# Optimization experiments

Hardware: AMD Instinct MI355X
Metric: run time of the kernel (lower is better)

Reference implementation:

```python
import jax, jax.numpy as jnp
import numpy as np

B, S, L, C, H, D, CP = 32, 4, 64, 32, 4, 8, 16  # batch, tracks, bins, c_msa, heads, d_head, c_pair


def _ln(x, g, b, eps=1e-5):
    m = jnp.mean(x, axis=-1, keepdims=True)
    v = jnp.mean((x - m) ** 2, axis=-1, keepdims=True)
    return (x - m) / jnp.sqrt(v + eps) * g + b


def setup_inputs() -> dict:
    key = jax.random.key(0)
    ks = jax.random.split(key, 20)
    n = lambda k, shape, s=0.1: jax.random.normal(k, shape, jnp.float32) * s
    return dict(
        chip_ctcf=n(ks[0], (B, L), 1.0),
        chip_hac=n(ks[1], (B, L), 1.0),
        chip_me1=n(ks[2], (B, L), 1.0),
        chip_me3=n(ks[3], (B, L), 1.0),
        bulk_map=n(ks[4], (B, 1, L, L), 1.0),
        we_w=n(ks[5], (C, 1)), we_b=jnp.zeros((C,), jnp.float32),
        pos=n(ks[6], (1, 1, L, C)),
        mn_g=jnp.ones((C,), jnp.float32), mn_b=jnp.zeros((C,), jnp.float32),
        wq=n(ks[7], (C, C)), bq=jnp.zeros((C,), jnp.float32),
        wk=n(ks[8], (C, C)), bk=jnp.zeros((C,), jnp.float32),
        wv=n(ks[9], (C, C)), bv=jnp.zeros((C,), jnp.float32),
        wo=n(ks[10], (C, C)), bo=jnp.zeros((C,), jnp.float32),
        an_g=jnp.ones((C,), jnp.float32), an_b=jnp.zeros((C,), jnp.float32),
        conv_w=n(ks[11], (H,)), conv_b=jnp.zeros((H,), jnp.float32),
        gate_w=n(ks[12], (H, D, D)), gate_b=jnp.zeros((H, D), jnp.float32),
        pp_w=n(ks[13], (CP, C * C), 0.03), pp_b=jnp.zeros((CP,), jnp.float32),
        ada_g=jnp.ones((CP,), jnp.float32), ada_b=jnp.zeros((CP,), jnp.float32),
        ada_alpha=jnp.ones((1,), jnp.float32),
    )


def reference(chip_ctcf, chip_hac, chip_me1, chip_me3, bulk_map,
              we_w, we_b, pos, mn_g, mn_b,
              wq, bq, wk, bk, wv, bv, wo, bo, an_g, an_b,
              conv_w, conv_b, gate_w, gate_b,
              pp_w, pp_b, ada_g, ada_b, ada_alpha):
    # 1) build MSA: (B, S=4, L, C)
    signals = jnp.stack([chip_ctcf, chip_hac, chip_me1, chip_me3], axis=1)  # (B,S,L)
    msa = signals[..., None] * we_w[:, 0] + we_b                            # Linear(1,C)
    x = _ln(msa + pos, mn_g, mn_b)                                          # (B,S,L,C)

    # 2) row self-attention with bulk-derived per-head bias
    q = (x @ wq.T + bq).reshape(B, S, L, H, D)
    k = (x @ wk.T + bk).reshape(B, S, L, H, D)
    v = (x @ wv.T + bv).reshape(B, S, L, H, D)
    scores = jnp.einsum('bslhd,bsmhd->bshlm', q, k) / jnp.sqrt(jnp.float32(D))
    bias = bulk_map * conv_w.reshape(1, H, 1, 1) + conv_b.reshape(1, H, 1, 1)  # 1x1 conv -> (B,H,L,L)
    attn = jax.nn.softmax(scores + bias[:, None], axis=-1)                     # (B,S,H,L,L)
    out = jnp.einsum('bshlm,bsmhd->bshld', attn, v)
    gate = jax.nn.sigmoid(jnp.einsum('hcd,bshld->bshlc', gate_w, out)
                          + gate_b[None, None, :, None, :])
    out = out * gate
    out = out.transpose(0, 1, 3, 2, 4).reshape(B, S, L, C)
    out = out @ wo.T + bo
    x = _ln(x + out, an_g, an_b)                                            # post-attn LayerNorm

    # 3) outer-product (of max over tracks) pair features
    m = jnp.max(x, axis=1)                                                  # (B,L,C)
    pair = jnp.einsum('bic,bjd->bijcd', m, m).reshape(B, L, L, C * C)       # (B,L,L,1024)
    nrm = jnp.sqrt(jnp.sum(pair * pair, axis=-1, keepdims=True))
    pair = pair / jnp.maximum(nrm, 1e-6)                                    # F.normalize
    feat = pair @ pp_w.T + pp_b                                             # (B,L,L,CP)
    feat = feat + ada_alpha * _ln(feat, ada_g, ada_b)                       # AdaNorm
    feat = jax.nn.silu(feat)
    return feat.transpose(0, 3, 1, 2)                                       # (B,CP,L,L)
```

## Files before the change

kernel.cpp:

```cpp
#include <hip/hip_runtime.h>
#include <hip/hip_bf16.h>

#define NB 32
#define NS 4
#define NL 64
#define NC 32
#define NH 4
#define ND 8
#define NCP 16

using fp = const float* __restrict__;

__global__ __launch_bounds__(512) void k1_attn(
    fp ctcf, fp hac, fp me1, fp me3, fp bulk,
    fp we_w, fp we_b, fp pos, fp mn_g, fp mn_b,
    fp wq, fp bq, fp wk, fp bk, fp wv, fp bv,
    fp wo, fp bo, fp an_g, fp an_b,
    fp conv_w, fp conv_b, fp gate_w, fp gate_b,
    float* __restrict__ xpostT)
{
    __shared__ __align__(16) float q2[NL*36];
    __shared__ __align__(16) float k2[NL*36];
    __shared__ __align__(16) float v2[NL*36];
    __shared__ __align__(16) float x2[NL*36];
    __shared__ __align__(16) float a2[NL*36];
    __shared__ float bs[32*65];
    __shared__ __align__(16) float ws_wq[NC*NC];
    __shared__ __align__(16) float ws_wk[NC*NC];
    __shared__ __align__(16) float ws_wv[NC*NC];
    __shared__ __align__(16) float ws_wo[NC*NC];
    __shared__ __align__(16) float ws_gw[NH*ND*ND];
    __shared__ __align__(16) float ws_par[352];

    const int t    = threadIdx.x;
    const int w    = t >> 6;
    const int l    = t & 63;
    const int bx   = blockIdx.x;
    const int b    = bx >> 3;
    const int s    = (bx >> 1) & 3;
    const int half = bx & 1;

    if (t < 256) ((float4*)ws_wq)[t]       = ((const float4*)wq)[t];
    else         ((float4*)ws_wk)[t - 256] = ((const float4*)wk)[t - 256];

    if (t < 256) ((float4*)ws_wv)[t] = ((const float4*)wv)[t];
    else {
        int u = t - 256;
        if (u < 64) ((float4*)ws_gw)[u] = ((const float4*)gate_w)[u];
        else if (u < 152){
            int p = u - 64;
            const float* sp = (p < 8)  ? we_w : (p < 16) ? we_b
                            : (p < 24) ? mn_g : (p < 32) ? mn_b
                            : (p < 40) ? bq   : (p < 48) ? bk
                            : (p < 56) ? bv   : (p < 64) ? bo
                            : (p < 72) ? an_g : (p < 80) ? an_b : gate_b;
            ((float4*)ws_par)[p] = ((const float4*)sp)[p & 7];
        }
    }
    if (t < 256){
        int c = t >> 3, k4 = t & 7;
        ((float4*)ws_wo)[c*8 + (k4 ^ ((c >> 1) & 7))] = ((const float4*)wo)[t];
    }
    {
        float4 v = ((const float4*)(bulk + b*NL*NL + half*32*NL))[t];
        int row = t >> 4, col = (t & 15) << 2;
        float* dst = &bs[row*65 + col];
        dst[0] = v.x; dst[1] = v.y; dst[2] = v.z; dst[3] = v.w;
    }

    fp sigp = (s == 0) ? ctcf : (s == 1) ? hac : (s == 2) ? me1 : me3;
    const float sig = sigp[b*NL + l];
    __syncthreads();

    const float4* pws = (const float4*)ws_par;

    float x[NC];
    float mean = 0.f;
#pragma unroll
    for (int k4 = 0; k4 < 8; k4++){
        float4 ww = pws[k4];
        float4 wb = pws[8 + k4];
        float4 pp = ((const float4*)pos)[l*8 + k4];
        x[4*k4+0] = sig*ww.x + wb.x + pp.x;
        x[4*k4+1] = sig*ww.y + wb.y + pp.y;
        x[4*k4+2] = sig*ww.z + wb.z + pp.z;
        x[4*k4+3] = sig*ww.w + wb.w + pp.w;
        mean += x[4*k4+0] + x[4*k4+1] + x[4*k4+2] + x[4*k4+3];
    }
    mean *= (1.f/NC);
    float var = 0.f;
#pragma unroll
    for (int c = 0; c < NC; c++){ float d = x[c] - mean; var += d*d; }
    var *= (1.f/NC);
    float inv = rsqrtf(var + 1e-5f);
#pragma unroll
    for (int k4 = 0; k4 < 8; k4++){
        float4 gg = pws[16 + k4];
        float4 bb = pws[24 + k4];
        x[4*k4+0] = (x[4*k4+0] - mean)*inv*gg.x + bb.x;
        x[4*k4+1] = (x[4*k4+1] - mean)*inv*gg.y + bb.y;
        x[4*k4+2] = (x[4*k4+2] - mean)*inv*gg.z + bb.z;
        x[4*k4+3] = (x[4*k4+3] - mean)*inv*gg.w + bb.w;
    }

    float aqv[4], akv[4], avv[4];
#pragma unroll
    for (int e4 = 0; e4 < 4; e4++){
        const int e = (w << 2) + e4;
        float aq = ws_par[128 + e], ak = ws_par[160 + e], av = ws_par[192 + e];
#pragma unroll
        for (int k4 = 0; k4 < 8; k4++){
            float4 wq4 = *(const float4*)&ws_wq[e*NC + 4*k4];
            float4 wk4 = *(const float4*)&ws_wk[e*NC + 4*k4];
            float4 wv4 = *(const float4*)&ws_wv[e*NC + 4*k4];
            float x0 = x[4*k4+0], x1 = x[4*k4+1], x2v = x[4*k4+2], x3 = x[4*k4+3];
            aq += wq4.x*x0 + wq4.y*x1 + wq4.z*x2v + wq4.w*x3;
            ak += wk4.x*x0 + wk4.y*x1 + wk4.z*x2v + wk4.w*x3;
            av += wv4.x*x0 + wv4.y*x1 + wv4.z*x2v + wv4.w*x3;
        }
        aqv[e4] = aq; akv[e4] = ak; avv[e4] = av;
    }
    {
        const int slt = ((w >> 1) ^ (l >> 4));
        const int kh  = (w & 1);
        const int off = l*36 + slt*8 + kh*4;
        *(float4*)&q2[off] = make_float4(aqv[0], aqv[1], aqv[2], aqv[3]);
        *(float4*)&k2[off] = make_float4(akv[0], akv[1], akv[2], akv[3]);
        *(float4*)&v2[off] = make_float4(avv[0], avv[1], avv[2], avv[3]);
        float xa = 0.f, xb2 = 0.f, xc = 0.f, xd = 0.f;
#pragma unroll
        for (int ww = 0; ww < 8; ww++)
            if (ww == w){ xa = x[4*ww]; xb2 = x[4*ww+1]; xc = x[4*ww+2]; xd = x[4*ww+3]; }
        *(float4*)&x2[l*36 + ((w ^ (l >> 4)) << 2)] = make_float4(xa, xb2, xc, xd);
    }
    __syncthreads();

    {
        const int h   = w >> 1;
        const int sub = ((w & 1) << 6) | l;
        const int rl  = sub >> 2;
        const int q4  = sub & 3;
        const int r   = half*32 + rl;
        const int m0  = q4 << 4;

        const int qoff = r*36 + ((h ^ (r >> 4)) << 3);
        float4 qa = *(const float4*)&q2[qoff];
        float4 qb = *(const float4*)&q2[qoff + 4];

        const float rs8 = 0.35355339059327373f;
        const float cw = conv_w[h], cb = conv_b[h];
        const float* bsr = &bs[rl*65];
        float srow[16];
        float mx = -1e30f;
#pragma unroll
        for (int mi = 0; mi < 16; mi++){
            int m  = m0 + mi;
            int kb = m*36 + ((h ^ (m >> 4)) << 3);
            float4 ka  = *(const float4*)&k2[kb];
            float4 kb4 = *(const float4*)&k2[kb + 4];
            float dot = qa.x*ka.x + qa.y*ka.y + qa.z*ka.z + qa.w*ka.w
                      + qb.x*kb4.x + qb.y*kb4.y + qb.z*kb4.z + qb.w*kb4.w;
            float vv = dot*rs8 + bsr[m]*cw + cb;
            srow[mi] = vv;
            mx = fmaxf(mx, vv);
        }
        mx = fmaxf(mx, __shfl_xor(mx, 1));
        mx = fmaxf(mx, __shfl_xor(mx, 2));
        float sm = 0.f;
#pragma unroll
        for (int mi = 0; mi < 16; mi++){ srow[mi] = __expf(srow[mi] - mx); sm += srow[mi]; }
        sm += __shfl_xor(sm, 1);
        sm += __shfl_xor(sm, 2);
        float is = 1.f / sm;

        float4 oa = make_float4(0.f,0.f,0.f,0.f);
        float4 ob = make_float4(0.f,0.f,0.f,0.f);
#pragma unroll
        for (int mi = 0; mi < 16; mi++){
            int m  = m0 + mi;
            int vb = m*36 + ((h ^ (m >> 4)) << 3);
            float a = srow[mi] * is;
            float4 va  = *(const float4*)&v2[vb];
            float4 vb4 = *(const float4*)&v2[vb + 4];
            oa.x += a*va.x;  oa.y += a*va.y;  oa.z += a*va.z;  oa.w += a*va.w;
            ob.x += a*vb4.x; ob.y += a*vb4.y; ob.z += a*vb4.z; ob.w += a*vb4.w;
        }
#define RED2(f) f += __shfl_xor(f, 1); f += __shfl_xor(f, 2);
        RED2(oa.x) RED2(oa.y) RED2(oa.z) RED2(oa.w)
        RED2(ob.x) RED2(ob.y) RED2(ob.z) RED2(ob.w)
#undef RED2

        const int c8l = q4 << 1;
        const float* gwl = &ws_gw[(h*ND + c8l)*ND];
        float4 g1 = *(const float4*)gwl;
        float4 g2 = *(const float4*)(gwl + 4);
        float4 g3 = *(const float4*)(gwl + 8);
        float4 g4 = *(const float4*)(gwl + 12);
        float gl = ws_par[320 + h*ND + c8l]
                 + g1.x*oa.x + g1.y*oa.y + g1.z*oa.z + g1.w*oa.w
                 + g2.x*ob.x + g2.y*ob.y + g2.z*ob.z + g2.w*ob.w;
        float gh = ws_par[320 + h*ND + c8l + 1]
                 + g3.x*oa.x + g3.y*oa.y + g3.z*oa.z + g3.w*oa.w
                 + g4.x*ob.x + g4.y*ob.y + g4.z*ob.z + g4.w*ob.w;
        float olo, ohi;
        if      (q4 == 0){ olo = oa.x; ohi = oa.y; }
        else if (q4 == 1){ olo = oa.z; ohi = oa.w; }
        else if (q4 == 2){ olo = ob.x; ohi = ob.y; }
        else             { olo = ob.z; ohi = ob.w; }
        float vlo = olo * (1.f/(1.f + __expf(-gl)));
        float vhi = ohi * (1.f/(1.f + __expf(-gh)));
        *(float2*)&a2[r*36 + h*8 + c8l] = make_float2(vlo, vhi);
    }
    __syncthreads();

    {
        const int rg = t >> 4;
        const int cg = t & 15;
        const int r3 = half*32 + rg;
        const int c0 = cg << 1;
        float accL = ws_par[224 + c0], accH = ws_par[224 + c0 + 1];
#pragma unroll
        for (int k4 = 0; k4 < 8; k4++){
            float4 av = *(const float4*)&a2[r3*36 + (k4 << 2)];
            float4 w1 = ((const float4*)ws_wo)[c0*8 + (k4 ^ (cg & 7))];
            float4 w2 = ((const float4*)ws_wo)[(c0 + 1)*8 + (k4 ^ (cg & 7))];
            accL += av.x*w1.x + av.y*w1.y + av.z*w1.z + av.w*w1.w;
            accH += av.x*w2.x + av.y*w2.y + av.z*w2.z + av.w*w2.w;
        }
        float2 xr = *(const float2*)&x2[r3*36 + (((cg >> 1) ^ (r3 >> 4)) << 2) + ((cg & 1) << 1)];
        float vlo = xr.x + accL;
        float vhi = xr.y + accH;
        float ps = vlo + vhi, pq = vlo*vlo + vhi*vhi;
        ps += __shfl_xor(ps, 1);  pq += __shfl_xor(pq, 1);
        ps += __shfl_xor(ps, 2);  pq += __shfl_xor(pq, 2);
        ps += __shfl_xor(ps, 4);  pq += __shfl_xor(pq, 4);
        ps += __shfl_xor(ps, 8);  pq += __shfl_xor(pq, 8);
        float mn = ps * (1.f/NC);
        float vr = pq * (1.f/NC) - mn*mn;
        float iv = rsqrtf(vr + 1e-5f);
        float2 og;
        og.x = (vlo - mn)*iv*ws_par[256 + c0]     + ws_par[288 + c0];
        og.y = (vhi - mn)*iv*ws_par[256 + c0 + 1] + ws_par[288 + c0 + 1];
        *(float2*)&xpostT[((b*NS + s)*NL + r3)*NC + c0] = og;
    }
}

__global__ __launch_bounds__(256) void k23_pair(
    const float* __restrict__ xpostT, fp pp_w,
    fp pp_b, fp ada_g, fp ada_b, fp ada_alpha,
    float* __restrict__ out)
{
    __shared__ float ppws[8*NC*NC];
    __shared__ float mh[NC*66];
    __shared__ float u[NCP*4*NC];
    __shared__ float nrm_s[NL];

    const int b  = blockIdx.x >> 4;
    const int it = blockIdx.x & 15;
    const int t  = threadIdx.x;
    const int w  = t >> 6;
    const int j  = t & 63;

    float4 s1[8];
#pragma unroll
    for (int k = 0; k < 8; k++) s1[k] = ((const float4*)pp_w)[k*256 + t];

    const float4* xb4 = (const float4*)(xpostT + b*NS*NL*NC);
#pragma unroll
    for (int k = 0; k < 2; k++){
        int idx = k*256 + t;
        float4 v0 = xb4[idx];
        float4 v1 = xb4[512  + idx];
        float4 v2 = xb4[1024 + idx];
        float4 v3 = xb4[1536 + idx];
        float m0 = fmaxf(fmaxf(v0.x, v1.x), fmaxf(v2.x, v3.x));
        float m1 = fmaxf(fmaxf(v0.y, v1.y), fmaxf(v2.y, v3.y));
        float m2 = fmaxf(fmaxf(v0.z, v1.z), fmaxf(v2.z, v3.z));
        float m3 = fmaxf(fmaxf(v0.w, v1.w), fmaxf(v2.w, v3.w));
        int l = idx >> 3, c4 = idx & 7;
        mh[(4*c4+0)*66 + l] = m0;
        mh[(4*c4+1)*66 + l] = m1;
        mh[(4*c4+2)*66 + l] = m2;
        mh[(4*c4+3)*66 + l] = m3;
    }
#pragma unroll
    for (int k = 0; k < 8; k++) ((float4*)ppws)[k*256 + t] = s1[k];
    __syncthreads();

    if (t < NL){
        float sq = 0.f;
#pragma unroll
        for (int c = 0; c < NC; c++){ float v = mh[c*66 + t]; sq += v*v; }
        nrm_s[t] = sqrtf(sq);
    }

    float4 s2[8];
#pragma unroll
    for (int k = 0; k < 8; k++) s2[k] = ((const float4*)pp_w)[2048 + k*256 + t];

#pragma unroll
    for (int loop = 0; loop < 4; loop++){
        int idx = loop*256 + t;
        int d  = idx & 31;
        int ip = (idx >> 5) & 3;
        int pl = idx >> 7;
        int i  = it*4 + ip;
        float acc = 0.f;
#pragma unroll
        for (int c = 0; c < NC; c++)
            acc += mh[c*66 + i] * ppws[pl*1024 + c*32 + d];
        u[pl*128 + ip*32 + d] = acc;
    }
    __syncthreads();
#pragma unroll
    for (int k = 0; k < 8; k++) ((float4*)ppws)[k*256 + t] = s2[k];
    __syncthreads();

#pragma unroll
    for (int loop = 0; loop < 4; loop++){
        int idx = loop*256 + t;
        int d  = idx & 31;
        int ip = (idx >> 5) & 3;
        int pl = idx >> 7;
        int i  = it*4 + ip;
        float acc = 0.f;
#pragma unroll
        for (int c = 0; c < NC; c++)
            acc += mh[c*66 + i] * ppws[pl*1024 + c*32 + d];
        u[(8 + pl)*128 + ip*32 + d] = acc;
    }
    __syncthreads();

    float md[NC];
#pragma unroll
    for (int c = 0; c < NC; c++) md[c] = mh[c*66 + j];

    const int i = it*4 + w;
    float f[NCP];
#pragma unroll
    for (int p = 0; p < NCP; p++){
        float a = 0.f;
#pragma unroll
        for (int k4 = 0; k4 < 8; k4++){
            float4 uv = *(const float4*)&u[p*128 + w*32 + (k4 << 2)];
            a += uv.x*md[4*k4+0] + uv.y*md[4*k4+1] + uv.z*md[4*k4+2] + uv.w*md[4*k4+3];
        }
        f[p] = a;
    }

    const float sc = 1.f / fmaxf(nrm_s[i] * nrm_s[j], 1e-6f);
    const float alpha = ada_alpha[0];
    float fsum = 0.f, fsq = 0.f;
#pragma unroll
    for (int p = 0; p < NCP; p++){
        float v = f[p]*sc + pp_b[p];
        f[p] = v; fsum += v; fsq += v*v;
    }
    float fmean = fsum * (1.f/NCP);
    float fvar  = fsq * (1.f/NCP) - fmean*fmean;
    float finv  = rsqrtf(fvar + 1e-5f);
#pragma unroll
    for (int p = 0; p < NCP; p++){
        float v = f[p] + alpha * ((f[p] - fmean)*finv*ada_g[p] + ada_b[p]);
        out[((b*NCP + p)*NL + i)*NL + j] = v / (1.f + __expf(-v));
    }
}

extern "C" void kernel_launch(void* const* d_in, const int* in_sizes, int n_in,
                              void* d_out, int out_size, void* d_ws, size_t ws_size,
                              hipStream_t stream)
{
    float* xpostT = (float*)d_ws;

    k1_attn<<<NB*NS*2, 512, 0, stream>>>(
        (fp)d_in[0], (fp)d_in[1], (fp)d_in[2], (fp)d_in[3], (fp)d_in[4],
        (fp)d_in[5], (fp)d_in[6], (fp)d_in[7], (fp)d_in[8], (fp)d_in[9],
        (fp)d_in[10], (fp)d_in[11], (fp)d_in[12], (fp)d_in[13], (fp)d_in[14], (fp)d_in[15],
        (fp)d_in[16], (fp)d_in[17], (fp)d_in[18], (fp)d_in[19],
        (fp)d_in[20], (fp)d_in[21], (fp)d_in[22], (fp)d_in[23], xpostT);

    k23_pair<<<NB*16, 256, 0, stream>>>(
        xpostT, (fp)d_in[24], (fp)d_in[25], (fp)d_in[26], (fp)d_in[27], (fp)d_in[28],
        (float*)d_out);
}
```

Baseline: 137.8 us.

## Fuse attention and pair kernels into one cooperative launch with grid sync

Merges the two kernels into a single cooperative kernel that shares one aliased shared-memory buffer. A grid-wide sync separates the attention phase from the pair-feature phase, and the pp_w weights are prefetched before the barrier. The pair phase is re-tiled for 512 threads over 256 blocks, so each block now handles 8 rows instead of 4. This removes the second launch and its gap, but adds grid-sync cost and requires all 256 blocks to be co-resident.

Result: slower. 271.7 us (+97.2%).

```diff
diff --git a/kernel.cpp b/kernel.cpp
--- a/kernel.cpp
+++ b/kernel.cpp
@@ -1,5 +1,6 @@
 #include <hip/hip_runtime.h>
 #include <hip/hip_bf16.h>
+#include <hip/hip_cooperative_groups.h>
 
 #define NB 32
 #define NS 4
@@ -11,26 +12,42 @@
 
 using fp = const float* __restrict__;
 
-__global__ __launch_bounds__(512) void k1_attn(
-    fp ctcf, fp hac, fp me1, fp me3, fp bulk,
-    fp we_w, fp we_b, fp pos, fp mn_g, fp mn_b,
-    fp wq, fp bq, fp wk, fp bk, fp wv, fp bv,
-    fp wo, fp bo, fp an_g, fp an_b,
-    fp conv_w, fp conv_b, fp gate_w, fp gate_b,
-    float* __restrict__ xpostT)
+struct KArgs {
+    const float* p[29];
+    float* xpostT;
+    float* out;
+};
+
+__global__ __launch_bounds__(512) void fused(KArgs A)
 {
-    __shared__ __align__(16) float q2[NL*36];
-    __shared__ __align__(16) float k2[NL*36];
-    __shared__ __align__(16) float v2[NL*36];
-    __shared__ __align__(16) float x2[NL*36];
-    __shared__ __align__(16) float a2[NL*36];
-    __shared__ float bs[32*65];
-    __shared__ __align__(16) float ws_wq[NC*NC];
-    __shared__ __align__(16) float ws_wk[NC*NC];
-    __shared__ __align__(16) float ws_wv[NC*NC];
-    __shared__ __align__(16) float ws_wo[NC*NC];
-    __shared__ __align__(16) float ws_gw[NH*ND*ND];
-    __shared__ __align__(16) float ws_par[352];
+    fp ctcf = A.p[0];  fp hac  = A.p[1];  fp me1  = A.p[2];  fp me3  = A.p[3];
+    fp bulk = A.p[4];  fp we_w = A.p[5];  fp we_b = A.p[6];  fp pos  = A.p[7];
+    fp mn_g = A.p[8];  fp mn_b = A.p[9];  fp wq   = A.p[10]; fp bq   = A.p[11];
+    fp wk   = A.p[12]; fp bk   = A.p[13]; fp wv   = A.p[14]; fp bv   = A.p[15];
+    fp wo   = A.p[16]; fp bo   = A.p[17]; fp an_g = A.p[18]; fp an_b = A.p[19];
+    fp conv_w = A.p[20]; fp conv_b = A.p[21]; fp gate_w = A.p[22]; fp gate_b = A.p[23];
+    fp pp_w = A.p[24]; fp pp_b = A.p[25]; fp ada_g = A.p[26]; fp ada_b = A.p[27];
+    fp ada_alpha = A.p[28];
+    float* __restrict__ xpostT = A.xpostT;
+    float* __restrict__ out    = A.out;
+
+    __shared__ __align__(16) float smem[18304];
+    float* q2     = smem;
+    float* k2     = smem + 2304;
+    float* v2     = smem + 4608;
+    float* x2     = smem + 6912;
+    float* a2     = smem + 9216;
+    float* bs     = smem + 11520;
+    float* ws_wq  = smem + 13600;
+    float* ws_wk  = smem + 14624;
+    float* ws_wv  = smem + 15648;
+    float* ws_wo  = smem + 16672;
+    float* ws_gw  = smem + 17696;
+    float* ws_par = smem + 17952;
+    float* ppws  = smem;
+    float* mh    = smem + 8192;
+    float* us    = smem + 10304;
+    float* nrm_s = smem + 14400;
 
     const int t    = threadIdx.x;
     const int w    = t >> 6;
@@ -103,24 +120,24 @@
         x[4*k4+3] = (x[4*k4+3] - mean)*inv*gg.w + bb.w;
     }
 
-    float aqv[4], akv[4], avv[4];
-#pragma unroll
-    for (int e4 = 0; e4 < 4; e4++){
-        const int e = (w << 2) + e4;
-        float aq = ws_par[128 + e], ak = ws_par[160 + e], av = ws_par[192 + e];
-#pragma unroll
-        for (int k4 = 0; k4 < 8; k4++){
-            float4 wq4 = *(const float4*)&ws_wq[e*NC + 4*k4];
-            float4 wk4 = *(const float4*)&ws_wk[e*NC + 4*k4];
-            float4 wv4 = *(const float4*)&ws_wv[e*NC + 4*k4];
-            float x0 = x[4*k4+0], x1 = x[4*k4+1], x2v = x[4*k4+2], x3 = x[4*k4+3];
-            aq += wq4.x*x0 + wq4.y*x1 + wq4.z*x2v + wq4.w*x3;
-            ak += wk4.x*x0 + wk4.y*x1 + wk4.z*x2v + wk4.w*x3;
-            av += wv4.x*x0 + wv4.y*x1 + wv4.z*x2v + wv4.w*x3;
-        }
-        aqv[e4] = aq; akv[e4] = ak; avv[e4] = av;
-    }
-    {
+    {
+        float aqv[4], akv[4], avv[4];
+#pragma unroll
+        for (int e4 = 0; e4 < 4; e4++){
+            const int e = (w << 2) + e4;
+            float aq = ws_par[128 + e], ak = ws_par[160 + e], av = ws_par[192 + e];
+#pragma unroll
+            for (int k4 = 0; k4 < 8; k4++){
+                float4 wq4 = *(const float4*)&ws_wq[e*NC + 4*k4];
+                float4 wk4 = *(const float4*)&ws_wk[e*NC + 4*k4];
+                float4 wv4 = *(const float4*)&ws_wv[e*NC + 4*k4];
+                float x0 = x[4*k4+0], x1 = x[4*k4+1], x2v = x[4*k4+2], x3 = x[4*k4+3];
+                aq += wq4.x*x0 + wq4.y*x1 + wq4.z*x2v + wq4.w*x3;
+                ak += wk4.x*x0 + wk4.y*x1 + wk4.z*x2v + wk4.w*x3;
+                av += wv4.x*x0 + wv4.y*x1 + wv4.z*x2v + wv4.w*x3;
+            }
+            aqv[e4] = aq; akv[e4] = ak; avv[e4] = av;
+        }
         const int slt = ((w >> 1) ^ (l >> 4));
         const int kh  = (w & 1);
         const int off = l*36 + slt*8 + kh*4;
@@ -243,48 +260,37 @@
         og.y = (vhi - mn)*iv*ws_par[256 + c0 + 1] + ws_par[288 + c0 + 1];
         *(float2*)&xpostT[((b*NS + s)*NL + r3)*NC + c0] = og;
     }
-}
-
-__global__ __launch_bounds__(256) void k23_pair(
-    const float* __restrict__ xpostT, fp pp_w,
-    fp pp_b, fp ada_g, fp ada_b, fp ada_alpha,
-    float* __restrict__ out)
-{
-    __shared__ float ppws[8*NC*NC];
-    __shared__ float mh[NC*66];
-    __shared__ float u[NCP*4*NC];
-    __shared__ float nrm_s[NL];
-
-    const int b  = blockIdx.x >> 4;
-    const int it = blockIdx.x & 15;
-    const int t  = threadIdx.x;
-    const int w  = t >> 6;
-    const int j  = t & 63;
-
-    float4 s1[8];
-#pragma unroll
-    for (int k = 0; k < 8; k++) s1[k] = ((const float4*)pp_w)[k*256 + t];
-
-    const float4* xb4 = (const float4*)(xpostT + b*NS*NL*NC);
-#pragma unroll
-    for (int k = 0; k < 2; k++){
-        int idx = k*256 + t;
-        float4 v0 = xb4[idx];
-        float4 v1 = xb4[512  + idx];
-        float4 v2 = xb4[1024 + idx];
-        float4 v3 = xb4[1536 + idx];
-        float m0 = fmaxf(fmaxf(v0.x, v1.x), fmaxf(v2.x, v3.x));
-        float m1 = fmaxf(fmaxf(v0.y, v1.y), fmaxf(v2.y, v3.y));
-        float m2 = fmaxf(fmaxf(v0.z, v1.z), fmaxf(v2.z, v3.z));
-        float m3 = fmaxf(fmaxf(v0.w, v1.w), fmaxf(v2.w, v3.w));
-        int l = idx >> 3, c4 = idx & 7;
-        mh[(4*c4+0)*66 + l] = m0;
-        mh[(4*c4+1)*66 + l] = m1;
-        mh[(4*c4+2)*66 + l] = m2;
-        mh[(4*c4+3)*66 + l] = m3;
-    }
-#pragma unroll
-    for (int k = 0; k < 8; k++) ((float4*)ppws)[k*256 + t] = s1[k];
+
+    float4 s1[4];
+    {
+        const float4* pp4 = (const float4*)pp_w;
+#pragma unroll
+        for (int k = 0; k < 4; k++) s1[k] = pp4[k*512 + t];
+    }
+
+    __threadfence();
+    cooperative_groups::this_grid().sync();
+
+    const int itp = bx & 7;
+
+    {
+        const float4* xb4 = (const float4*)(xpostT + b*NS*NL*NC);
+        float4 v0 = xb4[t];
+        float4 v1 = xb4[512  + t];
+        float4 v2l = xb4[1024 + t];
+        float4 v3 = xb4[1536 + t];
+        float m0 = fmaxf(fmaxf(v0.x, v1.x), fmaxf(v2l.x, v3.x));
+        float m1 = fmaxf(fmaxf(v0.y, v1.y), fmaxf(v2l.y, v3.y));
+        float m2 = fmaxf(fmaxf(v0.z, v1.z), fmaxf(v2l.z, v3.z));
+        float m3 = fmaxf(fmaxf(v0.w, v1.w), fmaxf(v2l.w, v3.w));
+        int ll = t >> 3, c4 = t & 7;
+        mh[(4*c4+0)*66 + ll] = m0;
+        mh[(4*c4+1)*66 + ll] = m1;
+        mh[(4*c4+2)*66 + ll] = m2;
+        mh[(4*c4+3)*66 + ll] = m3;
+    }
+#pragma unroll
+    for (int k = 0; k < 4; k++) ((float4*)ppws)[k*512 + t] = s1[k];
     __syncthreads();
 
     if (t < NL){
@@ -294,61 +300,64 @@
         nrm_s[t] = sqrtf(sq);
     }
 
-    float4 s2[8];
-#pragma unroll
-    for (int k = 0; k < 8; k++) s2[k] = ((const float4*)pp_w)[2048 + k*256 + t];
+    float4 s2[4];
+    {
+        const float4* pp4 = (const float4*)pp_w;
+#pragma unroll
+        for (int k = 0; k < 4; k++) s2[k] = pp4[2048 + k*512 + t];
+    }
 
 #pragma unroll
     for (int loop = 0; loop < 4; loop++){
-        int idx = loop*256 + t;
+        int idx = loop*512 + t;
         int d  = idx & 31;
-        int ip = (idx >> 5) & 3;
-        int pl = idx >> 7;
-        int i  = it*4 + ip;
+        int ii = (idx >> 5) & 7;
+        int pl = idx >> 8;
+        int i  = itp*8 + ii;
         float acc = 0.f;
 #pragma unroll
         for (int c = 0; c < NC; c++)
             acc += mh[c*66 + i] * ppws[pl*1024 + c*32 + d];
-        u[pl*128 + ip*32 + d] = acc;
-    }
-    __syncthreads();
-#pragma unroll
-    for (int k = 0; k < 8; k++) ((float4*)ppws)[k*256 + t] = s2[k];
+        us[pl*256 + ii*32 + d] = acc;
+    }
+    __syncthreads();
+#pragma unroll
+    for (int k = 0; k < 4; k++) ((float4*)ppws)[k*512 + t] = s2[k];
     __syncthreads();
 
 #pragma unroll
     for (int loop = 0; loop < 4; loop++){
-        int idx = loop*256 + t;
+        int idx = loop*512 + t;
         int d  = idx & 31;
-        int ip = (idx >> 5) & 3;
-        int pl = idx >> 7;
-        int i  = it*4 + ip;
+        int ii = (idx >> 5) & 7;
+        int pl = idx >> 8;
+        int i  = itp*8 + ii;
         float acc = 0.f;
 #pragma unroll
         for (int c = 0; c < NC; c++)
             acc += mh[c*66 + i] * ppws[pl*1024 + c*32 + d];
-        u[(8 + pl)*128 + ip*32 + d] = acc;
+        us[(8 + pl)*256 + ii*32 + d] = acc;
     }
     __syncthreads();
 
     float md[NC];
 #pragma unroll
-    for (int c = 0; c < NC; c++) md[c] = mh[c*66 + j];
-
-    const int i = it*4 + w;
+    for (int c = 0; c < NC; c++) md[c] = mh[c*66 + l];
+
+    const int i = itp*8 + w;
     float f[NCP];
 #pragma unroll
     for (int p = 0; p < NCP; p++){
         float a = 0.f;
 #pragma unroll
         for (int k4 = 0; k4 < 8; k4++){
-            float4 uv = *(const float4*)&u[p*128 + w*32 + (k4 << 2)];
+            float4 uv = *(const float4*)&us[p*256 + w*32 + (k4 << 2)];
             a += uv.x*md[4*k4+0] + uv.y*md[4*k4+1] + uv.z*md[4*k4+2] + uv.w*md[4*k4+3];
         }
         f[p] = a;
     }
 
-    const float sc = 1.f / fmaxf(nrm_s[i] * nrm_s[j], 1e-6f);
+    const float sc = 1.f / fmaxf(nrm_s[i] * nrm_s[l], 1e-6f);
     const float alpha = ada_alpha[0];
     float fsum = 0.f, fsq = 0.f;
 #pragma unroll
@@ -362,7 +371,7 @@
 #pragma unroll
     for (int p = 0; p < NCP; p++){
         float v = f[p] + alpha * ((f[p] - fmean)*finv*ada_g[p] + ada_b[p]);
-        out[((b*NCP + p)*NL + i)*NL + j] = v / (1.f + __expf(-v));
+        out[((b*NCP + p)*NL + i)*NL + l] = v / (1.f + __expf(-v));
     }
 }
 
@@ -370,16 +379,12 @@
                               void* d_out, int out_size, void* d_ws, size_t ws_size,
                               hipStream_t stream)
 {
-    float* xpostT = (float*)d_ws;
-
-    k1_attn<<<NB*NS*2, 512, 0, stream>>>(
-        (fp)d_in[0], (fp)d_in[1], (fp)d_in[2], (fp)d_in[3], (fp)d_in[4],
-        (fp)d_in[5], (fp)d_in[6], (fp)d_in[7], (fp)d_in[8], (fp)d_in[9],
-        (fp)d_in[10], (fp)d_in[11], (fp)d_in[12], (fp)d_in[13], (fp)d_in[14], (fp)d_in[15],
-        (fp)d_in[16], (fp)d_in[17], (fp)d_in[18], (fp)d_in[19],
-        (fp)d_in[20], (fp)d_in[21], (fp)d_in[22], (fp)d_in[23], xpostT);
-
-    k23_pair<<<NB*16, 256, 0, stream>>>(
-        xpostT, (fp)d_in[24], (fp)d_in[25], (fp)d_in[26], (fp)d_in[27], (fp)d_in[28],
-        (float*)d_out);
+    KArgs ka;
+    for (int i = 0; i < 29; i++) ka.p[i] = (const float*)d_in[i];
+    ka.xpostT = (float*)d_ws;
+    ka.out    = (float*)d_out;
+
+    void* kp[] = { &ka };
+    hipLaunchCooperativeKernel((const void*)fused, dim3(NB*NS*2), dim3(512),
+                               kp, 0, stream);
 }
```

## Split attention kernel into quarter-row blocks to double grid parallelism

Applied to the files above, without the earlier changes.

The attention kernel now assigns 16 query rows per block instead of 32, doubling the grid to 512 blocks. Each thread handles 8 keys instead of 16, with an extra shuffle stage in the softmax and output reductions. The gate and output-projection stages compute one channel per thread. More blocks should fill more CUs, but every block still recomputes the full LayerNorm and Q/K/V projection for all 64 positions and reloads all weights, which adds redundant work.

Result: slower. 144.8 us (+5.1%).

```diff
diff --git a/kernel.cpp b/kernel.cpp
--- a/kernel.cpp
+++ b/kernel.cpp
@@ -23,8 +23,8 @@
     __shared__ __align__(16) float k2[NL*36];
     __shared__ __align__(16) float v2[NL*36];
     __shared__ __align__(16) float x2[NL*36];
-    __shared__ __align__(16) float a2[NL*36];
-    __shared__ float bs[32*65];
+    __shared__ __align__(16) float a2[16*36];
+    __shared__ float bs[16*65];
     __shared__ __align__(16) float ws_wq[NC*NC];
     __shared__ __align__(16) float ws_wk[NC*NC];
     __shared__ __align__(16) float ws_wv[NC*NC];
@@ -36,9 +36,9 @@
     const int w    = t >> 6;
     const int l    = t & 63;
     const int bx   = blockIdx.x;
-    const int b    = bx >> 3;
-    const int s    = (bx >> 1) & 3;
-    const int half = bx & 1;
+    const int b    = bx >> 4;
+    const int s    = (bx >> 2) & 3;
+    const int qtr  = bx & 3;
 
     if (t < 256) ((float4*)ws_wq)[t]       = ((const float4*)wq)[t];
     else         ((float4*)ws_wk)[t - 256] = ((const float4*)wk)[t - 256];
@@ -61,8 +61,8 @@
         int c = t >> 3, k4 = t & 7;
         ((float4*)ws_wo)[c*8 + (k4 ^ ((c >> 1) & 7))] = ((const float4*)wo)[t];
     }
-    {
-        float4 v = ((const float4*)(bulk + b*NL*NL + half*32*NL))[t];
+    if (t < 256){
+        float4 v = ((const float4*)(bulk + b*NL*NL + qtr*16*NL))[t];
         int row = t >> 4, col = (t & 15) << 2;
         float* dst = &bs[row*65 + col];
         dst[0] = v.x; dst[1] = v.y; dst[2] = v.z; dst[3] = v.w;
@@ -103,24 +103,24 @@
         x[4*k4+3] = (x[4*k4+3] - mean)*inv*gg.w + bb.w;
     }
 
-    float aqv[4], akv[4], avv[4];
-#pragma unroll
-    for (int e4 = 0; e4 < 4; e4++){
-        const int e = (w << 2) + e4;
-        float aq = ws_par[128 + e], ak = ws_par[160 + e], av = ws_par[192 + e];
-#pragma unroll
-        for (int k4 = 0; k4 < 8; k4++){
-            float4 wq4 = *(const float4*)&ws_wq[e*NC + 4*k4];
-            float4 wk4 = *(const float4*)&ws_wk[e*NC + 4*k4];
-            float4 wv4 = *(const float4*)&ws_wv[e*NC + 4*k4];
-            float x0 = x[4*k4+0], x1 = x[4*k4+1], x2v = x[4*k4+2], x3 = x[4*k4+3];
-            aq += wq4.x*x0 + wq4.y*x1 + wq4.z*x2v + wq4.w*x3;
-            ak += wk4.x*x0 + wk4.y*x1 + wk4.z*x2v + wk4.w*x3;
-            av += wv4.x*x0 + wv4.y*x1 + wv4.z*x2v + wv4.w*x3;
-        }
-        aqv[e4] = aq; akv[e4] = ak; avv[e4] = av;
-    }
     {
+        float aqv[4], akv[4], avv[4];
+#pragma unroll
+        for (int e4 = 0; e4 < 4; e4++){
+            const int e = (w << 2) + e4;
+            float aq = ws_par[128 + e], ak = ws_par[160 + e], av = ws_par[192 + e];
+#pragma unroll
+            for (int k4 = 0; k4 < 8; k4++){
+                float4 wq4 = *(const float4*)&ws_wq[e*NC + 4*k4];
+                float4 wk4 = *(const float4*)&ws_wk[e*NC + 4*k4];
+                float4 wv4 = *(const float4*)&ws_wv[e*NC + 4*k4];
+                float x0 = x[4*k4+0], x1 = x[4*k4+1], x2v = x[4*k4+2], x3 = x[4*k4+3];
+                aq += wq4.x*x0 + wq4.y*x1 + wq4.z*x2v + wq4.w*x3;
+                ak += wk4.x*x0 + wk4.y*x1 + wk4.z*x2v + wk4.w*x3;
+                av += wv4.x*x0 + wv4.y*x1 + wv4.z*x2v + wv4.w*x3;
+            }
+            aqv[e4] = aq; akv[e4] = ak; avv[e4] = av;
+        }
         const int slt = ((w >> 1) ^ (l >> 4));
         const int kh  = (w & 1);
         const int off = l*36 + slt*8 + kh*4;
@@ -138,10 +138,10 @@
     {
         const int h   = w >> 1;
         const int sub = ((w & 1) << 6) | l;
-        const int rl  = sub >> 2;
-        const int q4  = sub & 3;
-        const int r   = half*32 + rl;
-        const int m0  = q4 << 4;
+        const int rl  = sub >> 3;
+        const int q8  = sub & 7;
+        const int r   = qtr*16 + rl;
+        const int m0  = q8 << 3;
 
         const int qoff = r*36 + ((h ^ (r >> 4)) << 3);
         float4 qa = *(const float4*)&q2[qoff];
@@ -150,10 +150,10 @@
         const float rs8 = 0.35355339059327373f;
         const float cw = conv_w[h], cb = conv_b[h];
         const float* bsr = &bs[rl*65];
-        float srow[16];
+        float srow[8];
         float mx = -1e30f;
 #pragma unroll
-        for (int mi = 0; mi < 16; mi++){
+        for (int mi = 0; mi < 8; mi++){
             int m  = m0 + mi;
             int kb = m*36 + ((h ^ (m >> 4)) << 3);
             float4 ka  = *(const float4*)&k2[kb];
@@ -166,17 +166,19 @@
         }
         mx = fmaxf(mx, __shfl_xor(mx, 1));
         mx = fmaxf(mx, __shfl_xor(mx, 2));
+        mx = fmaxf(mx, __shfl_xor(mx, 4));
         float sm = 0.f;
 #pragma unroll
-        for (int mi = 0; mi < 16; mi++){ srow[mi] = __expf(srow[mi] - mx); sm += srow[mi]; }
+        for (int mi = 0; mi < 8; mi++){ srow[mi] = __expf(srow[mi] - mx); sm += srow[mi]; }
         sm += __shfl_xor(sm, 1);
         sm += __shfl_xor(sm, 2);
+        sm += __shfl_xor(sm, 4);
         float is = 1.f / sm;
 
         float4 oa = make_float4(0.f,0.f,0.f,0.f);
         float4 ob = make_float4(0.f,0.f,0.f,0.f);
 #pragma unroll
-        for (int mi = 0; mi < 16; mi++){
+        for (int mi = 0; mi < 8; mi++){
             int m  = m0 + mi;
             int vb = m*36 + ((h ^ (m >> 4)) << 3);
             float a = srow[mi] * is;
@@ -185,63 +187,53 @@
             oa.x += a*va.x;  oa.y += a*va.y;  oa.z += a*va.z;  oa.w += a*va.w;
             ob.x += a*vb4.x; ob.y += a*vb4.y; ob.z += a*vb4.z; ob.w += a*vb4.w;
         }
-#define RED2(f) f += __shfl_xor(f, 1); f += __shfl_xor(f, 2);
-        RED2(oa.x) RED2(oa.y) RED2(oa.z) RED2(oa.w)
-        RED2(ob.x) RED2(ob.y) RED2(ob.z) RED2(ob.w)
-#undef RED2
-
-        const int c8l = q4 << 1;
-        const float* gwl = &ws_gw[(h*ND + c8l)*ND];
+#define RED3(f) f += __shfl_xor(f, 1); f += __shfl_xor(f, 2); f += __shfl_xor(f, 4);
+        RED3(oa.x) RED3(oa.y) RED3(oa.z) RED3(oa.w)
+        RED3(ob.x) RED3(ob.y) RED3(ob.z) RED3(ob.w)
+#undef RED3
+
+        const float* gwl = &ws_gw[(h*ND + q8)*ND];
         float4 g1 = *(const float4*)gwl;
         float4 g2 = *(const float4*)(gwl + 4);
-        float4 g3 = *(const float4*)(gwl + 8);
-        float4 g4 = *(const float4*)(gwl + 12);
-        float gl = ws_par[320 + h*ND + c8l]
-                 + g1.x*oa.x + g1.y*oa.y + g1.z*oa.z + g1.w*oa.w
-                 + g2.x*ob.x + g2.y*ob.y + g2.z*ob.z + g2.w*ob.w;
-        float gh = ws_par[320 + h*ND + c8l + 1]
-                 + g3.x*oa.x + g3.y*oa.y + g3.z*oa.z + g3.w*oa.w
-                 + g4.x*ob.x + g4.y*ob.y + g4.z*ob.z + g4.w*ob.w;
-        float olo, ohi;
-        if      (q4 == 0){ olo = oa.x; ohi = oa.y; }
-        else if (q4 == 1){ olo = oa.z; ohi = oa.w; }
-        else if (q4 == 2){ olo = ob.x; ohi = ob.y; }
-        else             { olo = ob.z; ohi = ob.w; }
-        float vlo = olo * (1.f/(1.f + __expf(-gl)));
-        float vhi = ohi * (1.f/(1.f + __expf(-gh)));
-        *(float2*)&a2[r*36 + h*8 + c8l] = make_float2(vlo, vhi);
+        float g = ws_par[320 + h*ND + q8]
+                + g1.x*oa.x + g1.y*oa.y + g1.z*oa.z + g1.w*oa.w
+                + g2.x*ob.x + g2.y*ob.y + g2.z*ob.z + g2.w*ob.w;
+        float oc = oa.x;
+        if (q8 == 1) oc = oa.y;
+        if (q8 == 2) oc = oa.z;
+        if (q8 == 3) oc = oa.w;
+        if (q8 == 4) oc = ob.x;
+        if (q8 == 5) oc = ob.y;
+        if (q8 == 6) oc = ob.z;
+        if (q8 == 7) oc = ob.w;
+        a2[rl*36 + h*8 + q8] = oc * (1.f/(1.f + __expf(-g)));
     }
     __syncthreads();
 
     {
-        const int rg = t >> 4;
-        const int cg = t & 15;
-        const int r3 = half*32 + rg;
-        const int c0 = cg << 1;
-        float accL = ws_par[224 + c0], accH = ws_par[224 + c0 + 1];
+        const int r3 = t >> 5;
+        const int c  = t & 31;
+        const int rg = qtr*16 + r3;
+        float acc = ws_par[224 + c];
 #pragma unroll
         for (int k4 = 0; k4 < 8; k4++){
             float4 av = *(const float4*)&a2[r3*36 + (k4 << 2)];
-            float4 w1 = ((const float4*)ws_wo)[c0*8 + (k4 ^ (cg & 7))];
-            float4 w2 = ((const float4*)ws_wo)[(c0 + 1)*8 + (k4 ^ (cg & 7))];
-            accL += av.x*w1.x + av.y*w1.y + av.z*w1.z + av.w*w1.w;
-            accH += av.x*w2.x + av.y*w2.y + av.z*w2.z + av.w*w2.w;
-        }
-        float2 xr = *(const float2*)&x2[r3*36 + (((cg >> 1) ^ (r3 >> 4)) << 2) + ((cg & 1) << 1)];
-        float vlo = xr.x + accL;
-        float vhi = xr.y + accH;
-        float ps = vlo + vhi, pq = vlo*vlo + vhi*vhi;
+            float4 w1 = ((const float4*)ws_wo)[c*8 + (k4 ^ ((c >> 1) & 7))];
+            acc += av.x*w1.x + av.y*w1.y + av.z*w1.z + av.w*w1.w;
+        }
+        float xr = x2[rg*36 + (((c >> 2) ^ (rg >> 4)) << 2) + (c & 3)];
+        float val = xr + acc;
+        float ps = val, pq = val*val;
         ps += __shfl_xor(ps, 1);  pq += __shfl_xor(pq, 1);
         ps += __shfl_xor(ps, 2);  pq += __shfl_xor(pq, 2);
         ps += __shfl_xor(ps, 4);  pq += __shfl_xor(pq, 4);
         ps += __shfl_xor(ps, 8);  pq += __shfl_xor(pq, 8);
+        ps += __shfl_xor(ps, 16); pq += __shfl_xor(pq, 16);
         float mn = ps * (1.f/NC);
         float vr = pq * (1.f/NC) - mn*mn;
         float iv = rsqrtf(vr + 1e-5f);
-        float2 og;
-        og.x = (vlo - mn)*iv*ws_par[256 + c0]     + ws_par[288 + c0];
-        og.y = (vhi - mn)*iv*ws_par[256 + c0 + 1] + ws_par[288 + c0 + 1];
-        *(float2*)&xpostT[((b*NS + s)*NL + r3)*NC + c0] = og;
+        xpostT[((b*NS + s)*NL + rg)*NC + c] =
+            (val - mn)*iv*ws_par[256 + c] + ws_par[288 + c];
     }
 }
 
@@ -372,7 +364,7 @@
 {
     float* xpostT = (float*)d_ws;
 
-    k1_attn<<<NB*NS*2, 512, 0, stream>>>(
+    k1_attn<<<NB*NS*4, 512, 0, stream>>>(
         (fp)d_in[0], (fp)d_in[1], (fp)d_in[2], (fp)d_in[3], (fp)d_in[4],
         (fp)d_in[5], (fp)d_in[6], (fp)d_in[7], (fp)d_in[8], (fp)d_in[9],
         (fp)d_in[10], (fp)d_in[11], (fp)d_in[12], (fp)d_in[13], (fp)d_in[14], (fp)d_in[15],
```
